# Optimization experiments

Measured on AMD Instinct MI355X. Metric: run time of the kernel, lower is better.

The kernel has to match this reference:

```python
import jax, jax.numpy as jnp
import numpy as np

N_EDGE = 1_000_000
N_NODE = 100_000
EDGE_DIM = 64
N_RADIAL = 16
UP_DIM = 256


def silu(x):
    return x * jax.nn.sigmoid(x)  # Swish(beta=1.0)


def setup_inputs() -> dict:
    key = jax.random.key(0)
    ks = jax.random.split(key, 12)
    s = 0.05
    return {
        "x": jax.random.normal(ks[0], (N_EDGE, EDGE_DIM), jnp.float32),
        "rbf": jax.random.normal(ks[1], (N_EDGE, N_RADIAL), jnp.float32),
        "idx_i": jax.random.randint(ks[2], (N_EDGE,), 0, N_NODE, jnp.int32).astype(jnp.int64),
        "num_nodes": N_NODE,
        "W_rbf": jax.random.normal(ks[3], (N_RADIAL, EDGE_DIM), jnp.float32) * s,
        "W_up": jax.random.normal(ks[4], (EDGE_DIM, UP_DIM), jnp.float32) * s,
        "W1": jax.random.normal(ks[5], (UP_DIM, UP_DIM), jnp.float32) * s,
        "b1": jnp.zeros((UP_DIM,), jnp.float32),
        "W2": jax.random.normal(ks[6], (UP_DIM, UP_DIM), jnp.float32) * s,
        "b2": jnp.zeros((UP_DIM,), jnp.float32),
        "W3": jax.random.normal(ks[7], (UP_DIM, UP_DIM), jnp.float32) * s,
        "b3": jnp.zeros((UP_DIM,), jnp.float32),
        "W_out": jax.random.normal(ks[8], (UP_DIM, 1), jnp.float32) * s,
    }


def reference(x, rbf, idx_i, num_nodes, W_rbf, W_up, W1, b1, W2, b2, W3, b3, W_out):
    # Gate edge embeddings by rbf projection, scatter-add to center nodes.
    e = (rbf @ W_rbf) * x                              # (n_edge, edge_dim)
    h = jax.ops.segment_sum(e, idx_i, num_segments=num_nodes)  # (n_node, edge_dim)
    h = h @ W_up                                       # (n_node, up_dim)
    h = silu(h @ W1 + b1)
    h = silu(h @ W2 + b2)
    h = silu(h @ W3 + b3)
    return h @ W_out                                   # (n_node, out_dim)
```

## Files before the change

### kernel.cpp

```cpp
#include <hip/hip_runtime.h>
#include <hip/hip_bf16.h>

#define EDGE_DIM 64
#define UPD 256

typedef __attribute__((ext_vector_type(8))) short bf16x8;
typedef __attribute__((ext_vector_type(4))) float f32x4;

__device__ __forceinline__ short f2bf(float v) {
    __hip_bfloat16 b = __float2bfloat16(v);
    return *(short*)&b;
}
__device__ __forceinline__ float bf2f(short s) {
    __hip_bfloat16 b = *(__hip_bfloat16*)&s;
    return __bfloat162float(b);
}

__device__ __forceinline__ void split_trunc(float v, short& hi, short& lo) {
    unsigned u = __float_as_uint(v);
    unsigned hu = u & 0xFFFF0000u;
    hi = (short)(hu >> 16);
    float rem = v - __uint_as_float(hu);
    lo = (short)(__float_as_uint(rem) >> 16);
}

__global__ __launch_bounds__(256) void zero_ws_kernel(
    float4* __restrict__ h4, long long n4, int* __restrict__ count, int nn) {
    const long long t = (long long)blockIdx.x * blockDim.x + threadIdx.x;
    const long long stride = (long long)gridDim.x * blockDim.x;
    const float4 z = {0.f, 0.f, 0.f, 0.f};
    for (long long i = t; i < n4; i += stride) h4[i] = z;
    for (long long i = t; i < nn; i += stride) count[i] = 0;
}

__device__ __forceinline__ int detect_use64_block(const void* idx_v,
                                                  int n_edge, int nn,
                                                  int* bad_s) {
    if (threadIdx.x == 0) *bad_s = 0;
    __syncthreads();
    const long long* p = (const long long*)idx_v;
    int i = threadIdx.x;
    if (i < 256 && i < n_edge) {
        long long v = p[i];
        if (v < 0 || v >= (long long)nn) *bad_s = 1;
    }
    __syncthreads();
    return !(*bad_s);
}

__global__ __launch_bounds__(256) void count_kernel(
    const void* __restrict__ idx_v, int n_edge, int nn,
    int* __restrict__ count) {
    __shared__ int bad_s;
    const int use64 = detect_use64_block(idx_v, n_edge, nn, &bad_s);
    const int t = blockIdx.x * blockDim.x + threadIdx.x;
    const int nt = gridDim.x * blockDim.x;
    const int n4 = n_edge >> 2;
    if (use64) {
        const longlong2* p2 = (const longlong2*)idx_v;
        for (int i = t; i < n4; i += nt) {
            longlong2 a = p2[i * 2], b = p2[i * 2 + 1];
            atomicAdd(&count[(int)a.x], 1);
            atomicAdd(&count[(int)a.y], 1);
            atomicAdd(&count[(int)b.x], 1);
            atomicAdd(&count[(int)b.y], 1);
        }
        const long long* p = (const long long*)idx_v;
        for (int e = n4 * 4 + t; e < n_edge; e += nt)
            atomicAdd(&count[(int)p[e]], 1);
    } else {
        const int4* p4 = (const int4*)idx_v;
        for (int i = t; i < n4; i += nt) {
            int4 v = p4[i];
            atomicAdd(&count[v.x], 1);
            atomicAdd(&count[v.y], 1);
            atomicAdd(&count[v.z], 1);
            atomicAdd(&count[v.w], 1);
        }
        const int* p = (const int*)idx_v;
        for (int e = n4 * 4 + t; e < n_edge; e += nt)
            atomicAdd(&count[p[e]], 1);
    }
}

__global__ __launch_bounds__(256) void scan_a(const int* __restrict__ count,
                                              int* __restrict__ base,
                                              int* __restrict__ partial,
                                              int nn) {
    __shared__ int s[256];
    const int tid = threadIdx.x;
    const int i0 = blockIdx.x * 1024 + tid * 4;
    int c[4], tsum = 0;
#pragma unroll
    for (int j = 0; j < 4; ++j) {
        c[j] = (i0 + j < nn) ? count[i0 + j] : 0;
        tsum += c[j];
    }
    s[tid] = tsum;
    __syncthreads();
    for (int off = 1; off < 256; off <<= 1) {
        int v = (tid >= off) ? s[tid - off] : 0;
        __syncthreads();
        s[tid] += v;
        __syncthreads();
    }
    int run = s[tid] - tsum;
    if (tid == 255) partial[blockIdx.x] = s[255];
#pragma unroll
    for (int j = 0; j < 4; ++j) {
        if (i0 + j < nn) base[i0 + j] = run;
        run += c[j];
    }
}

__global__ __launch_bounds__(256) void scan_b(int* __restrict__ partial,
                                              int nblk) {
    __shared__ int s[256];
    const int tid = threadIdx.x;
    int v = (tid < nblk) ? partial[tid] : 0;
    s[tid] = v;
    __syncthreads();
    for (int off = 1; off < 256; off <<= 1) {
        int u = (tid >= off) ? s[tid - off] : 0;
        __syncthreads();
        s[tid] += u;
        __syncthreads();
    }
    if (tid < nblk) partial[tid] = s[tid] - v;
}

__global__ __launch_bounds__(256) void scan_c(int* __restrict__ base,
                                              int* __restrict__ cursor,
                                              const int* __restrict__ partial,
                                              int nn, int n_edge) {
    const int tid = threadIdx.x;
    const int b = blockIdx.x;
    const int add = partial[b];
    const int i0 = b * 1024 + tid * 4;
#pragma unroll
    for (int j = 0; j < 4; ++j) {
        int i = i0 + j;
        if (i < nn) {
            int v = base[i] + add;
            base[i] = v;
            cursor[i] = v;
        }
    }
    if (b == 0 && tid == 0) base[nn] = n_edge;
}

__global__ __launch_bounds__(256) void fill_order_kernel(
    const void* __restrict__ idx_v, int n_edge, int nn,
    int* __restrict__ cursor, int2* __restrict__ ordnode) {
    __shared__ int bad_s;
    const int use64 = detect_use64_block(idx_v, n_edge, nn, &bad_s);
    const int t = blockIdx.x * blockDim.x + threadIdx.x;
    const int nt = gridDim.x * blockDim.x;
    const int n4 = n_edge >> 2;
    if (use64) {
        const longlong2* p2 = (const longlong2*)idx_v;
        for (int i = t; i < n4; i += nt) {
            longlong2 a = p2[i * 2], b = p2[i * 2 + 1];
            int e0 = i * 4;
            int nd;
            nd = (int)a.x;
            ordnode[atomicAdd(&cursor[nd], 1)] = make_int2(e0 + 0, nd);
            nd = (int)a.y;
            ordnode[atomicAdd(&cursor[nd], 1)] = make_int2(e0 + 1, nd);
            nd = (int)b.x;
            ordnode[atomicAdd(&cursor[nd], 1)] = make_int2(e0 + 2, nd);
            nd = (int)b.y;
            ordnode[atomicAdd(&cursor[nd], 1)] = make_int2(e0 + 3, nd);
        }
        const long long* p = (const long long*)idx_v;
        for (int e = n4 * 4 + t; e < n_edge; e += nt) {
            int nd = (int)p[e];
            ordnode[atomicAdd(&cursor[nd], 1)] = make_int2(e, nd);
        }
    } else {
        const int4* p4 = (const int4*)idx_v;
        for (int i = t; i < n4; i += nt) {
            int4 v = p4[i];
            int e0 = i * 4;
            ordnode[atomicAdd(&cursor[v.x], 1)] = make_int2(e0 + 0, v.x);
            ordnode[atomicAdd(&cursor[v.y], 1)] = make_int2(e0 + 1, v.y);
            ordnode[atomicAdd(&cursor[v.z], 1)] = make_int2(e0 + 2, v.z);
            ordnode[atomicAdd(&cursor[v.w], 1)] = make_int2(e0 + 3, v.w);
        }
        const int* p = (const int*)idx_v;
        for (int e = n4 * 4 + t; e < n_edge; e += nt) {
            int nd = p[e];
            ordnode[atomicAdd(&cursor[nd], 1)] = make_int2(e, nd);
        }
    }
}

#define SEG_ISSUE(G, E, XV, RV)                                      \
    {                                                                \
        const int j0_ = (G) * 16;                                    \
        _Pragma("unroll") for (int j = 0; j < 16; ++j) {             \
            E[j] = __builtin_amdgcn_readlane(ev, j0_ + j);           \
            XV[j] = x[(size_t)E[j] * EDGE_DIM + lane];               \
            RV[j] = rbf[(size_t)E[j] * 16 + (lane & 15)];            \
        }                                                            \
    }

#define SEG_CONSUME(G, XV, RV)                                       \
    {                                                                \
        const int j0_ = (G) * 16;                                    \
        _Pragma("unroll") for (int j = 0; j < 16; ++j) {             \
            float gate = 0.f;                                        \
            _Pragma("unroll") for (int q = 0; q < 16; ++q) {         \
                int rb =                                             \
                    __builtin_amdgcn_readlane(__float_as_int(RV[j]), q); \
                gate = fmaf(__int_as_float(rb), wreg[q], gate);      \
            }                                                        \
            const int nd = __builtin_amdgcn_readlane(ndv, j0_ + j);  \
            if (s0 + j0_ + j < n_edge) {                             \
                if (nd != cur) {                                     \
                    if (cur >= 0)                                    \
                        atomicAdd(&h[(size_t)cur * EDGE_DIM + lane], acc); \
                    cur = nd;                                        \
                    acc = 0.f;                                       \
                }                                                    \
                acc = fmaf(gate, XV[j], acc);                        \
            }                                                        \
        }                                                            \
    }

__global__ __launch_bounds__(256) void segsum3_kernel(
    const float* __restrict__ x, const float* __restrict__ rbf,
    const int2* __restrict__ ordnode, const float* __restrict__ Wrbf,
    float* __restrict__ h, int n_edge) {
    const int lane = threadIdx.x & 63;
    float wreg[16];
#pragma unroll
    for (int q = 0; q < 16; ++q) wreg[q] = Wrbf[q * EDGE_DIM + lane];

    const int wid = threadIdx.x >> 6;
    const int nchunks = (n_edge + 63) >> 6;
    const int stride = gridDim.x * 4;

    for (int c = blockIdx.x * 4 + wid; c < nchunks; c += stride) {
        const int s0 = c * 64;
        int slot = s0 + lane;
        if (slot >= n_edge) slot = n_edge - 1;
        const int2 on = ordnode[slot];
        const int ev = on.x;
        const int ndv = on.y;

        float acc = 0.f;
        int cur = -1;
        int eA[16], eB[16];
        float xvA[16], xvB[16], rvA[16], rvB[16];

        SEG_ISSUE(0, eA, xvA, rvA);
        SEG_ISSUE(1, eB, xvB, rvB);
        SEG_CONSUME(0, xvA, rvA);
        SEG_ISSUE(2, eA, xvA, rvA);
        SEG_CONSUME(1, xvB, rvB);
        SEG_ISSUE(3, eB, xvB, rvB);
        SEG_CONSUME(2, xvA, rvA);
        SEG_CONSUME(3, xvB, rvB);

        if (cur >= 0) atomicAdd(&h[(size_t)cur * EDGE_DIM + lane], acc);
    }
}

__device__ __forceinline__ void pack_body(const float* __restrict__ W,
                                          short* __restrict__ out, int t) {
    int l = t & 63, f = t >> 6;
    int kt = f >> 4, nt = f & 15;
    int kbase = kt * 32 + (l >> 4) * 8;
    int col = nt * 16 + (l & 15);
#pragma unroll
    for (int j = 0; j < 8; ++j) {
        float v = W[(kbase + j) * UPD + col];
        short hb = f2bf(v);
        short lb = f2bf(v - bf2f(hb));
        out[f * 1024 + l * 8 + j] = hb;
        out[f * 1024 + 512 + l * 8 + j] = lb;
    }
}

__global__ __launch_bounds__(256) void pack_all_kernel(
    const float* __restrict__ Wup, const float* __restrict__ W1,
    const float* __restrict__ W2, const float* __restrict__ W3,
    short* __restrict__ oup, short* __restrict__ o1, short* __restrict__ o2,
    short* __restrict__ o3) {
    const int b = blockIdx.x;
    if (b < 8) {
        pack_body(Wup, oup, b * 256 + threadIdx.x);
    } else if (b < 40) {
        pack_body(W1, o1, (b - 8) * 256 + threadIdx.x);
    } else if (b < 72) {
        pack_body(W2, o2, (b - 40) * 256 + threadIdx.x);
    } else {
        pack_body(W3, o3, (b - 72) * 256 + threadIdx.x);
    }
}

template <int NK>
__device__ __forceinline__ void mm_layer(const short* AH, const short* AL,
                                         const short* __restrict__ Wpk,
                                         int lr, int lh, int lane, int wq,
                                         f32x4 acc[4][4]) {
    bf16x8 bc[4][2];
#pragma unroll
    for (int nf = 0; nf < 4; ++nf) {
        const short* p = Wpk + (wq * 4 + nf) * 1024 + lane * 8;
        bc[nf][0] = *(const bf16x8*)(p);
        bc[nf][1] = *(const bf16x8*)(p + 512);
    }
#pragma unroll
    for (int kt = 0; kt < NK; ++kt) {
        bf16x8 a[4][2];
#pragma unroll
        for (int m = 0; m < 4; ++m) {
            int r = m * 16 + lr;
            int ch = (kt * 4 + lh) ^ (r & 7);
            int off = r * 256 + ch * 8;
            a[m][0] = *(const bf16x8*)(AH + off);
            a[m][1] = *(const bf16x8*)(AL + off);
        }
        bf16x8 bn[4][2];
        if (kt + 1 < NK) {
#pragma unroll
            for (int nf = 0; nf < 4; ++nf) {
                const short* p =
                    Wpk + ((kt + 1) * 16 + wq * 4 + nf) * 1024 + lane * 8;
                bn[nf][0] = *(const bf16x8*)(p);
                bn[nf][1] = *(const bf16x8*)(p + 512);
            }
        }
#pragma unroll
        for (int m = 0; m < 4; ++m)
#pragma unroll
            for (int nf = 0; nf < 4; ++nf)
                acc[m][nf] = __builtin_amdgcn_mfma_f32_16x16x32_bf16(
                    a[m][0], bc[nf][0], acc[m][nf], 0, 0, 0);
#pragma unroll
        for (int m = 0; m < 4; ++m)
#pragma unroll
            for (int nf = 0; nf < 4; ++nf)
                acc[m][nf] = __builtin_amdgcn_mfma_f32_16x16x32_bf16(
                    a[m][0], bc[nf][1], acc[m][nf], 0, 0, 0);
#pragma unroll
        for (int m = 0; m < 4; ++m)
#pragma unroll
            for (int nf = 0; nf < 4; ++nf)
                acc[m][nf] = __builtin_amdgcn_mfma_f32_16x16x32_bf16(
                    a[m][1], bc[nf][0], acc[m][nf], 0, 0, 0);
        if (kt + 1 < NK) {
#pragma unroll
            for (int nf = 0; nf < 4; ++nf) {
                bc[nf][0] = bn[nf][0];
                bc[nf][1] = bn[nf][1];
            }
        }
    }
}

template <bool ACT>
__device__ __forceinline__ void epilogue_store(f32x4 acc[4][4], short* AH,
                                               short* AL,
                                               const float* __restrict__ bias,
                                               int lr, int lh, int wq) {
    float bv[4] = {0.f, 0.f, 0.f, 0.f};
    if (bias) {
#pragma unroll
        for (int nf = 0; nf < 4; ++nf) bv[nf] = bias[wq * 64 + nf * 16 + lr];
    }
#pragma unroll
    for (int m = 0; m < 4; ++m)
#pragma unroll
        for (int nf = 0; nf < 4; ++nf) {
            int c = wq * 64 + nf * 16 + lr;
#pragma unroll
            for (int reg = 0; reg < 4; ++reg) {
                float v = acc[m][nf][reg] + bv[nf];
                if (ACT) {
                    float e = __expf(-v);
                    v = v * __builtin_amdgcn_rcpf(1.f + e);
                }
                int r = m * 16 + lh * 4 + reg;
                short hb, lb;
                split_trunc(v, hb, lb);
                int off = r * 256 + (((c >> 3) ^ (r & 7)) * 8) + (c & 7);
                AH[off] = hb;
                AL[off] = lb;
            }
        }
}

__global__ __launch_bounds__(256, 2) void node_mlp_mfma(
    const float* __restrict__ h,
    const short* __restrict__ Wup_pk, const short* __restrict__ W1_pk,
    const short* __restrict__ W2_pk, const short* __restrict__ W3_pk,
    const float* __restrict__ b1, const float* __restrict__ b2,
    const float* __restrict__ b3, const float* __restrict__ W_out,
    float* __restrict__ out, int nn) {
    __shared__ short AH[64 * 256];
    __shared__ short AL[64 * 256];
    __shared__ float Bpart[64 * 4];

    const int tid = threadIdx.x;
    const int lane = tid & 63, wq = tid >> 6;
    const int lr = lane & 15, lh = lane >> 4;
    const int node0 = blockIdx.x * 64;

#pragma unroll
    for (int i = 0; i < 4; ++i) {
        int idx4 = tid + i * 256;
        int r = idx4 >> 4, c4 = idx4 & 15;
        float4 v = {0.f, 0.f, 0.f, 0.f};
        if (node0 + r < nn)
            v = *(const float4*)(h + (size_t)(node0 + r) * EDGE_DIM + c4 * 4);
        short h0, h1, h2, h3, l0, l1, l2, l3;
        split_trunc(v.x, h0, l0);
        split_trunc(v.y, h1, l1);
        split_trunc(v.z, h2, l2);
        split_trunc(v.w, h3, l3);
        int off = r * 256 + (((c4 >> 1) ^ (r & 7)) * 8) + (c4 & 1) * 4;
        uint2 hw, lw;
        hw.x = (unsigned short)h0 | ((unsigned)(unsigned short)h1 << 16);
        hw.y = (unsigned short)h2 | ((unsigned)(unsigned short)h3 << 16);
        lw.x = (unsigned short)l0 | ((unsigned)(unsigned short)l1 << 16);
        lw.y = (unsigned short)l2 | ((unsigned)(unsigned short)l3 << 16);
        *(uint2*)(AH + off) = hw;
        *(uint2*)(AL + off) = lw;
    }
    __syncthreads();

    f32x4 acc[4][4];

#pragma unroll
    for (int m = 0; m < 4; ++m)
#pragma unroll
        for (int n = 0; n < 4; ++n) acc[m][n] = (f32x4){0.f, 0.f, 0.f, 0.f};
    mm_layer<2>(AH, AL, Wup_pk, lr, lh, lane, wq, acc);
    __syncthreads();
    epilogue_store<false>(acc, AH, AL, nullptr, lr, lh, wq);
    __syncthreads();

#pragma unroll
    for (int m = 0; m < 4; ++m)
#pragma unroll
        for (int n = 0; n < 4; ++n) acc[m][n] = (f32x4){0.f, 0.f, 0.f, 0.f};
    mm_layer<8>(AH, AL, W1_pk, lr, lh, lane, wq, acc);
    __syncthreads();
    epilogue_store<true>(acc, AH, AL, b1, lr, lh, wq);
    __syncthreads();

#pragma unroll
    for (int m = 0; m < 4; ++m)
#pragma unroll
        for (int n = 0; n < 4; ++n) acc[m][n] = (f32x4){0.f, 0.f, 0.f, 0.f};
    mm_layer<8>(AH, AL, W2_pk, lr, lh, lane, wq, acc);
    __syncthreads();
    epilogue_store<true>(acc, AH, AL, b2, lr, lh, wq);
    __syncthreads();

#pragma unroll
    for (int m = 0; m < 4; ++m)
#pragma unroll
        for (int n = 0; n < 4; ++n) acc[m][n] = (f32x4){0.f, 0.f, 0.f, 0.f};
    mm_layer<8>(AH, AL, W3_pk, lr, lh, lane, wq, acc);

    float b3v[4], wo[4];
#pragma unroll
    for (int nf = 0; nf < 4; ++nf) {
        int c = wq * 64 + nf * 16 + lr;
        b3v[nf] = b3[c];
        wo[nf] = W_out[c];
    }
#pragma unroll
    for (int m = 0; m < 4; ++m) {
#pragma unroll
        for (int reg = 0; reg < 4; ++reg) {
            float s = 0.f;
#pragma unroll
            for (int nf = 0; nf < 4; ++nf) {
                float v = acc[m][nf][reg] + b3v[nf];
                float e = __expf(-v);
                v = v * __builtin_amdgcn_rcpf(1.f + e);
                s = fmaf(v, wo[nf], s);
            }
            s += __shfl_xor(s, 1);
            s += __shfl_xor(s, 2);
            s += __shfl_xor(s, 4);
            s += __shfl_xor(s, 8);
            if (lr == 0) Bpart[(m * 16 + lh * 4 + reg) * 4 + wq] = s;
        }
    }
    __syncthreads();
    if (tid < 64) {
        float s = Bpart[tid * 4] + Bpart[tid * 4 + 1] + Bpart[tid * 4 + 2] +
                  Bpart[tid * 4 + 3];
        if (node0 + tid < nn) out[node0 + tid] = s;
    }
}

extern "C" void kernel_launch(void* const* d_in, const int* in_sizes, int n_in,
                              void* d_out, int out_size, void* d_ws, size_t ws_size,
                              hipStream_t stream) {
    const float* x     = (const float*)d_in[0];
    const float* rbf   = (const float*)d_in[1];
    const void*  idx   = d_in[2];
    const float* W_rbf = (const float*)d_in[4];
    const float* W_up  = (const float*)d_in[5];
    const float* W1    = (const float*)d_in[6];
    const float* b1    = (const float*)d_in[7];
    const float* W2    = (const float*)d_in[8];
    const float* b2    = (const float*)d_in[9];
    const float* W3    = (const float*)d_in[10];
    const float* b3    = (const float*)d_in[11];
    const float* W_out = (const float*)d_in[12];
    float* out = (float*)d_out;

    const int n_edge = in_sizes[0] / EDGE_DIM;
    const int nn = out_size;

    char* p = (char*)d_ws;
    float* h = (float*)p;            p += (size_t)nn * EDGE_DIM * sizeof(float);
    short* wup_pk = (short*)p;       p += 32 * 1024 * sizeof(short);
    short* w1_pk = (short*)p;        p += 128 * 1024 * sizeof(short);
    short* w2_pk = (short*)p;        p += 128 * 1024 * sizeof(short);
    short* w3_pk = (short*)p;        p += 128 * 1024 * sizeof(short);
    int* count = (int*)p;            p += (size_t)nn * sizeof(int);
    int* base = (int*)p;             p += (size_t)(nn + 1) * sizeof(int) + 12;
    int* cursor = (int*)p;           p += (size_t)nn * sizeof(int);
    int* partial = (int*)p;          p += 1024;
    int2* ordnode = (int2*)p;

    const int nblk_scan = (nn + 1023) / 1024;

    zero_ws_kernel<<<2048, 256, 0, stream>>>(
        (float4*)h, (long long)nn * EDGE_DIM / 4, count, nn);
    pack_all_kernel<<<104, 256, 0, stream>>>(W_up, W1, W2, W3, wup_pk, w1_pk,
                                             w2_pk, w3_pk);
    count_kernel<<<2048, 256, 0, stream>>>(idx, n_edge, nn, count);
    scan_a<<<nblk_scan, 256, 0, stream>>>(count, base, partial, nn);
    scan_b<<<1, 256, 0, stream>>>(partial, nblk_scan);
    scan_c<<<nblk_scan, 256, 0, stream>>>(base, cursor, partial, nn, n_edge);
    fill_order_kernel<<<2048, 256, 0, stream>>>(idx, n_edge, nn, cursor,
                                                ordnode);
    const int nchunks = (n_edge + 63) / 64;
    const int nblk_seg = (nchunks + 3) / 4;
    segsum3_kernel<<<nblk_seg, 256, 0, stream>>>(x, rbf, ordnode, W_rbf, h,
                                                 n_edge);

    const int nb = (nn + 63) / 64;
    node_mlp_mfma<<<nb, 256, 0, stream>>>(h, wup_pk, w1_pk, w2_pk, w3_pk,
                                          b1, b2, b3, W_out, out, nn);
}
```

Before: 354.3 us.

## Enlarge node MLP tile to 128 rows and simplify segment-sum load pipelining

The node MLP kernel now processes 128 nodes per block with 512 threads arranged as a 2x4 wave grid. Each packed weight fragment fetched from global memory is reused across twice as many rows, at the cost of double the LDS (about 128KB) and a single block per CU. The segment-sum kernel drops its explicit double-buffered issue/consume macros in favour of a plain per-group load-then-compute loop. That cuts register pressure but leaves any cross-group overlap to the compiler.

```diff
diff --git a/kernel.cpp b/kernel.cpp
--- a/kernel.cpp
+++ b/kernel.cpp
@@ -195,40 +195,7 @@
     }
 }
 
-#define SEG_ISSUE(G, E, XV, RV)                                      \
-    {                                                                \
-        const int j0_ = (G) * 16;                                    \
-        _Pragma("unroll") for (int j = 0; j < 16; ++j) {             \
-            E[j] = __builtin_amdgcn_readlane(ev, j0_ + j);           \
-            XV[j] = x[(size_t)E[j] * EDGE_DIM + lane];               \
-            RV[j] = rbf[(size_t)E[j] * 16 + (lane & 15)];            \
-        }                                                            \
-    }
-
-#define SEG_CONSUME(G, XV, RV)                                       \
-    {                                                                \
-        const int j0_ = (G) * 16;                                    \
-        _Pragma("unroll") for (int j = 0; j < 16; ++j) {             \
-            float gate = 0.f;                                        \
-            _Pragma("unroll") for (int q = 0; q < 16; ++q) {         \
-                int rb =                                             \
-                    __builtin_amdgcn_readlane(__float_as_int(RV[j]), q); \
-                gate = fmaf(__int_as_float(rb), wreg[q], gate);      \
-            }                                                        \
-            const int nd = __builtin_amdgcn_readlane(ndv, j0_ + j);  \
-            if (s0 + j0_ + j < n_edge) {                             \
-                if (nd != cur) {                                     \
-                    if (cur >= 0)                                    \
-                        atomicAdd(&h[(size_t)cur * EDGE_DIM + lane], acc); \
-                    cur = nd;                                        \
-                    acc = 0.f;                                       \
-                }                                                    \
-                acc = fmaf(gate, XV[j], acc);                        \
-            }                                                        \
-        }                                                            \
-    }
-
-__global__ __launch_bounds__(256) void segsum3_kernel(
+__global__ __launch_bounds__(256) void segsum2_kernel(
     const float* __restrict__ x, const float* __restrict__ rbf,
     const int2* __restrict__ ordnode, const float* __restrict__ Wrbf,
     float* __restrict__ h, int n_edge) {
@@ -251,18 +218,38 @@
 
         float acc = 0.f;
         int cur = -1;
-        int eA[16], eB[16];
-        float xvA[16], xvB[16], rvA[16], rvB[16];
-
-        SEG_ISSUE(0, eA, xvA, rvA);
-        SEG_ISSUE(1, eB, xvB, rvB);
-        SEG_CONSUME(0, xvA, rvA);
-        SEG_ISSUE(2, eA, xvA, rvA);
-        SEG_CONSUME(1, xvB, rvB);
-        SEG_ISSUE(3, eB, xvB, rvB);
-        SEG_CONSUME(2, xvA, rvA);
-        SEG_CONSUME(3, xvB, rvB);
-
+#pragma unroll
+        for (int g = 0; g < 4; ++g) {
+            const int j0 = g * 16;
+            int e[16];
+            float xv[16], rv[16];
+#pragma unroll
+            for (int j = 0; j < 16; ++j) {
+                e[j] = __builtin_amdgcn_readlane(ev, j0 + j);
+                xv[j] = x[(size_t)e[j] * EDGE_DIM + lane];
+                rv[j] = rbf[(size_t)e[j] * 16 + (lane & 15)];
+            }
+#pragma unroll
+            for (int j = 0; j < 16; ++j) {
+                float gate = 0.f;
+#pragma unroll
+                for (int q = 0; q < 16; ++q) {
+                    int rb = __builtin_amdgcn_readlane(
+                        __float_as_int(rv[j]), q);
+                    gate = fmaf(__int_as_float(rb), wreg[q], gate);
+                }
+                const int nd = __builtin_amdgcn_readlane(ndv, j0 + j);
+                if (s0 + j0 + j < n_edge) {
+                    if (nd != cur) {
+                        if (cur >= 0)
+                            atomicAdd(&h[(size_t)cur * EDGE_DIM + lane], acc);
+                        cur = nd;
+                        acc = 0.f;
+                    }
+                    acc = fmaf(gate, xv[j], acc);
+                }
+            }
+        }
         if (cur >= 0) atomicAdd(&h[(size_t)cur * EDGE_DIM + lane], acc);
     }
 }
@@ -303,12 +290,12 @@
 template <int NK>
 __device__ __forceinline__ void mm_layer(const short* AH, const short* AL,
                                          const short* __restrict__ Wpk,
-                                         int lr, int lh, int lane, int wq,
-                                         f32x4 acc[4][4]) {
+                                         int lr, int lh, int lane, int wrow,
+                                         int wcol, f32x4 acc[4][4]) {
     bf16x8 bc[4][2];
 #pragma unroll
     for (int nf = 0; nf < 4; ++nf) {
-        const short* p = Wpk + (wq * 4 + nf) * 1024 + lane * 8;
+        const short* p = Wpk + (wcol * 4 + nf) * 1024 + lane * 8;
         bc[nf][0] = *(const bf16x8*)(p);
         bc[nf][1] = *(const bf16x8*)(p + 512);
     }
@@ -317,7 +304,7 @@
         bf16x8 a[4][2];
 #pragma unroll
         for (int m = 0; m < 4; ++m) {
-            int r = m * 16 + lr;
+            int r = wrow * 64 + m * 16 + lr;
             int ch = (kt * 4 + lh) ^ (r & 7);
             int off = r * 256 + ch * 8;
             a[m][0] = *(const bf16x8*)(AH + off);
@@ -328,7 +315,7 @@
 #pragma unroll
             for (int nf = 0; nf < 4; ++nf) {
                 const short* p =
-                    Wpk + ((kt + 1) * 16 + wq * 4 + nf) * 1024 + lane * 8;
+                    Wpk + ((kt + 1) * 16 + wcol * 4 + nf) * 1024 + lane * 8;
                 bn[nf][0] = *(const bf16x8*)(p);
                 bn[nf][1] = *(const bf16x8*)(p + 512);
             }
@@ -365,17 +352,19 @@
 __device__ __forceinline__ void epilogue_store(f32x4 acc[4][4], short* AH,
                                                short* AL,
                                                const float* __restrict__ bias,
-                                               int lr, int lh, int wq) {
+                                               int lr, int lh, int wrow,
+                                               int wcol) {
     float bv[4] = {0.f, 0.f, 0.f, 0.f};
     if (bias) {
 #pragma unroll
-        for (int nf = 0; nf < 4; ++nf) bv[nf] = bias[wq * 64 + nf * 16 + lr];
+        for (int nf = 0; nf < 4; ++nf)
+            bv[nf] = bias[wcol * 64 + nf * 16 + lr];
     }
 #pragma unroll
     for (int m = 0; m < 4; ++m)
 #pragma unroll
         for (int nf = 0; nf < 4; ++nf) {
-            int c = wq * 64 + nf * 16 + lr;
+            int c = wcol * 64 + nf * 16 + lr;
 #pragma unroll
             for (int reg = 0; reg < 4; ++reg) {
                 float v = acc[m][nf][reg] + bv[nf];
@@ -383,7 +372,7 @@
                     float e = __expf(-v);
                     v = v * __builtin_amdgcn_rcpf(1.f + e);
                 }
-                int r = m * 16 + lh * 4 + reg;
+                int r = wrow * 64 + m * 16 + lh * 4 + reg;
                 short hb, lb;
                 split_trunc(v, hb, lb);
                 int off = r * 256 + (((c >> 3) ^ (r & 7)) * 8) + (c & 7);
@@ -393,25 +382,28 @@
         }
 }
 
-__global__ __launch_bounds__(256, 2) void node_mlp_mfma(
+__global__ __launch_bounds__(512, 1) void node_mlp_mfma(
     const float* __restrict__ h,
     const short* __restrict__ Wup_pk, const short* __restrict__ W1_pk,
     const short* __restrict__ W2_pk, const short* __restrict__ W3_pk,
     const float* __restrict__ b1, const float* __restrict__ b2,
     const float* __restrict__ b3, const float* __restrict__ W_out,
     float* __restrict__ out, int nn) {
-    __shared__ short AH[64 * 256];
-    __shared__ short AL[64 * 256];
-    __shared__ float Bpart[64 * 4];
+    __shared__ short AH[128 * 256];
+    __shared__ short AL[128 * 256];
+    __shared__ float Bpart[128 * 4];
 
     const int tid = threadIdx.x;
-    const int lane = tid & 63, wq = tid >> 6;
+    const int lane = tid & 63;
+    const int w = tid >> 6;
+    const int wrow = w >> 2;
+    const int wcol = w & 3;
     const int lr = lane & 15, lh = lane >> 4;
-    const int node0 = blockIdx.x * 64;
+    const int node0 = blockIdx.x * 128;
 
 #pragma unroll
     for (int i = 0; i < 4; ++i) {
-        int idx4 = tid + i * 256;
+        int idx4 = tid + i * 512;
         int r = idx4 >> 4, c4 = idx4 & 15;
         float4 v = {0.f, 0.f, 0.f, 0.f};
         if (node0 + r < nn)
@@ -438,39 +430,39 @@
     for (int m = 0; m < 4; ++m)
 #pragma unroll
         for (int n = 0; n < 4; ++n) acc[m][n] = (f32x4){0.f, 0.f, 0.f, 0.f};
-    mm_layer<2>(AH, AL, Wup_pk, lr, lh, lane, wq, acc);
-    __syncthreads();
-    epilogue_store<false>(acc, AH, AL, nullptr, lr, lh, wq);
+    mm_layer<2>(AH, AL, Wup_pk, lr, lh, lane, wrow, wcol, acc);
+    __syncthreads();
+    epilogue_store<false>(acc, AH, AL, nullptr, lr, lh, wrow, wcol);
     __syncthreads();
 
 #pragma unroll
     for (int m = 0; m < 4; ++m)
 #pragma unroll
         for (int n = 0; n < 4; ++n) acc[m][n] = (f32x4){0.f, 0.f, 0.f, 0.f};
-    mm_layer<8>(AH, AL, W1_pk, lr, lh, lane, wq, acc);
-    __syncthreads();
-    epilogue_store<true>(acc, AH, AL, b1, lr, lh, wq);
+    mm_layer<8>(AH, AL, W1_pk, lr, lh, lane, wrow, wcol, acc);
+    __syncthreads();
+    epilogue_store<true>(acc, AH, AL, b1, lr, lh, wrow, wcol);
     __syncthreads();
 
 #pragma unroll
     for (int m = 0; m < 4; ++m)
 #pragma unroll
         for (int n = 0; n < 4; ++n) acc[m][n] = (f32x4){0.f, 0.f, 0.f, 0.f};
-    mm_layer<8>(AH, AL, W2_pk, lr, lh, lane, wq, acc);
-    __syncthreads();
-    epilogue_store<true>(acc, AH, AL, b2, lr, lh, wq);
+    mm_layer<8>(AH, AL, W2_pk, lr, lh, lane, wrow, wcol, acc);
+    __syncthreads();
+    epilogue_store<true>(acc, AH, AL, b2, lr, lh, wrow, wcol);
     __syncthreads();
 
 #pragma unroll
     for (int m = 0; m < 4; ++m)
 #pragma unroll
         for (int n = 0; n < 4; ++n) acc[m][n] = (f32x4){0.f, 0.f, 0.f, 0.f};
-    mm_layer<8>(AH, AL, W3_pk, lr, lh, lane, wq, acc);
+    mm_layer<8>(AH, AL, W3_pk, lr, lh, lane, wrow, wcol, acc);
 
     float b3v[4], wo[4];
 #pragma unroll
     for (int nf = 0; nf < 4; ++nf) {
-        int c = wq * 64 + nf * 16 + lr;
+        int c = wcol * 64 + nf * 16 + lr;
         b3v[nf] = b3[c];
         wo[nf] = W_out[c];
     }
@@ -490,11 +482,14 @@
             s += __shfl_xor(s, 2);
             s += __shfl_xor(s, 4);
             s += __shfl_xor(s, 8);
-            if (lr == 0) Bpart[(m * 16 + lh * 4 + reg) * 4 + wq] = s;
-        }
-    }
-    __syncthreads();
-    if (tid < 64) {
+            if (lr == 0) {
+                int r = wrow * 64 + m * 16 + lh * 4 + reg;
+                Bpart[r * 4 + wcol] = s;
+            }
+        }
+    }
+    __syncthreads();
+    if (tid < 128) {
         float s = Bpart[tid * 4] + Bpart[tid * 4 + 1] + Bpart[tid * 4 + 2] +
                   Bpart[tid * 4 + 3];
         if (node0 + tid < nn) out[node0 + tid] = s;
@@ -547,10 +542,10 @@
                                                 ordnode);
     const int nchunks = (n_edge + 63) / 64;
     const int nblk_seg = (nchunks + 3) / 4;
-    segsum3_kernel<<<nblk_seg, 256, 0, stream>>>(x, rbf, ordnode, W_rbf, h,
+    segsum2_kernel<<<nblk_seg, 256, 0, stream>>>(x, rbf, ordnode, W_rbf, h,
                                                  n_edge);
 
-    const int nb = (nn + 63) / 64;
-    node_mlp_mfma<<<nb, 256, 0, stream>>>(h, wup_pk, w1_pk, w2_pk, w3_pk,
+    const int nb = (nn + 127) / 128;
+    node_mlp_mfma<<<nb, 512, 0, stream>>>(h, wup_pk, w1_pk, w2_pk, w3_pk,
                                           b1, b2, b3, W_out, out, nn);
 }
```

Result: slower. 374.3 us (+5.7%).
